# Performance work log

Measured on AMD Instinct MI355X. Metric: run time of the kernel, lower is better.

Reference implementation:

```python
import jax, jax.numpy as jnp
import numpy as np

ANNEALING_SCALE = 0.1
BS, NV, S, D, V = 2, 16, 1024, 768, 50257

def setup_inputs() -> dict:
    key = jax.random.key(0)
    k1, k2, k3, k4, k5 = jax.random.split(key, 5)
    return {
        "input_ids": jax.random.randint(k1, (BS, S), 0, V),
        "content": jax.random.normal(k2, (BS, NV, S, D), dtype=jnp.float32),
        "contextualization": jax.random.normal(k3, (BS, NV, S, S), dtype=jnp.float32) * 0.05,
        "lm_head_weight": jax.random.normal(k4, (V, D), dtype=jnp.float32) * 0.02,
        "content_weights": jax.random.uniform(k5, (V, NV), dtype=jnp.float32),
    }

def reference(input_ids, content, contextualization, lm_head_weight, content_weights):
    bs, nv, s, d = content.shape
    # --- mask_annealing ---
    # Original computes relu(content @ W.T) over full vocab then gathers at input_ids.
    # Equivalent: gather rows of W first, then contract (same math since relu is
    # elementwise and only gathered columns are summed).
    Wg = lm_head_weight[input_ids]                              # (bs, s, d)
    sims = jnp.einsum('bkid,bjd->bkij', content, Wg)            # (bs, 16, s, s)
    sims = jnp.sum(jax.nn.relu(sims), axis=3)                   # (bs, 16, s)
    scores = jax.nn.sigmoid(-ANNEALING_SCALE * sims + 6.0)
    # upweight_nearby modifier
    scores = scores * (1.0 + jnp.arange(s, dtype=content.dtype) / 100.0)[None, None, :]
    scores = jnp.transpose(scores, (0, 2, 1))                   # (bs, s, 16)
    # --- create_content_soft_mask ---
    cw = content_weights[input_ids]                             # (bs, s, 16)
    weights = cw * scores + (1.0 - scores)                      # (bs, s, 16)
    # --- weighted sense combination ---
    content_m = content * jnp.transpose(weights, (0, 2, 1))[..., None]  # (bs,16,s,d)
    hidden = jnp.einsum('bkij,bkjd->bid', contextualization, content_m) # (bs, s, d)
    logits = hidden @ lm_head_weight.T                          # (bs, s, vocab)
    return logits
```

## Files before the change

### kernel.cpp

```cpp
#include <hip/hip_runtime.h>
#include <cstdint>
#include <cstddef>

#define BSZ 2
#define NV 16
#define SEQ 1024
#define DIM 768
#define VOC 50257
#define VOCP 50304

typedef unsigned int u32;
typedef unsigned short u16;
typedef _Float16 half8 __attribute__((ext_vector_type(8)));
typedef float f32x4 __attribute__((ext_vector_type(4)));

__device__ __forceinline__ u16 f2h(float f) {
  return __builtin_bit_cast(unsigned short, (_Float16)f);
}
__device__ __forceinline__ u32 pk2h(float a, float b) {
  return (u32)f2h(a) | ((u32)f2h(b) << 16);
}

__device__ __forceinline__ void gload16(const u16* g, u16* l) {
  __builtin_amdgcn_global_load_lds(
      (const __attribute__((address_space(1))) void*)g,
      (__attribute__((address_space(3))) void*)l, 16, 0, 0);
}

__global__ void k_prep_content(const float* __restrict__ content,
                               u16* __restrict__ cbf, u16* __restrict__ cT) {
  __shared__ u16 tile[32][33];
  const int bk = blockIdx.z;
  const int d0 = blockIdx.x * 32, j0 = blockIdx.y * 32;
  const float* src = content + (size_t)bk * SEQ * DIM;
  u16* dst = cbf + (size_t)bk * SEQ * DIM;
  u16* dstT = cT + (size_t)bk * DIM * SEQ;
  const int c = threadIdx.x;
#pragma unroll
  for (int rr = 0; rr < 4; ++rr) {
    const int r = threadIdx.y * 4 + rr;
    const float v = src[(size_t)(j0 + r) * DIM + d0 + c];
    const u16 bv = f2h(v);
    dst[(size_t)(j0 + r) * DIM + d0 + c] = bv;
    tile[r][c] = bv;
  }
  __syncthreads();
#pragma unroll
  for (int rr = 0; rr < 4; ++rr) {
    const int r = threadIdx.y * 4 + rr;
    dstT[(size_t)(d0 + r) * SEQ + j0 + c] = tile[c][r];
  }
}

__global__ void k_prep_w(const float* __restrict__ W, u16* __restrict__ Wb) {
  const int v = blockIdx.x;
  const int c = threadIdx.x * 4;
  u32 lo, hi;
  if (v < VOC) {
    const float4 f = *(const float4*)(W + (size_t)v * DIM + c);
    lo = pk2h(f.x, f.y); hi = pk2h(f.z, f.w);
  } else {
    lo = 0u; hi = 0u;
  }
  *(uint2*)(Wb + (size_t)v * DIM + c) = make_uint2(lo, hi);
}

__global__ void k_gather(const int* __restrict__ ids, const u16* __restrict__ Wb,
                         u16* __restrict__ Wg) {
  const int b = blockIdx.y, j = blockIdx.x;
  const int row = ids[b * SEQ + j];
  const int c = threadIdx.x * 4;
  *(uint2*)(Wg + ((size_t)b * SEQ + j) * DIM + c) =
      *(const uint2*)(Wb + (size_t)row * DIM + c);
}

__global__ void k_zero(float* __restrict__ p, int n) {
  const int i = blockIdx.x * 256 + threadIdx.x;
  if (i < n) p[i] = 0.f;
}

template <int LDA, int LDB>
__device__ __forceinline__ void gemm_core(const u16* __restrict__ A,
                                          const u16* __restrict__ B, int ksteps,
                                          u16* As, u16* Bs, f32x4 (&acc)[4][4],
                                          int t) {
  const int lane = t & 63, w = t >> 6, wr = w >> 1, wc = w & 1;
  const int rl = lane & 15;
  const int gsw = (((lane >> 4) ^ ((rl >> 1) & 3)) * 8);
  const int srow = 16 * w + (lane >> 2);
  const int sg = (((lane & 3) ^ ((lane >> 3) & 3)) * 8);
  const size_t gaBase = (size_t)srow * LDA + sg;
  const size_t gbBase = (size_t)srow * LDB + sg;
  u16* lA = As + w * 512;
  u16* lB = Bs + w * 512;

#define STAGE_(bb, kt)                                                  \
  {                                                                     \
    const u16* ga_ = A + gaBase + (size_t)(kt) * 32;                    \
    const u16* gb_ = B + gbBase + (size_t)(kt) * 32;                    \
    gload16(ga_, lA + (bb) * 4096);                                     \
    gload16(ga_ + (size_t)64 * LDA, lA + (bb) * 4096 + 2048);           \
    gload16(gb_, lB + (bb) * 4096);                                     \
    gload16(gb_ + (size_t)64 * LDB, lB + (bb) * 4096 + 2048);           \
  }

#define FRAGS_(bb)                                                      \
  half8 af[4], bf[4];                                                   \
  _Pragma("unroll") for (int m = 0; m < 4; ++m)                         \
      af[m] = *(const half8*)(As + (bb) * 4096 +                        \
                              (wr * 64 + m * 16 + rl) * 32 + gsw);      \
  _Pragma("unroll") for (int n = 0; n < 4; ++n)                         \
      bf[n] = *(const half8*)(Bs + (bb) * 4096 +                        \
                              (wc * 64 + n * 16 + rl) * 32 + gsw);      \
  _Pragma("unroll") for (int m = 0; m < 4; ++m)                         \
      _Pragma("unroll") for (int n = 0; n < 4; ++n)                     \
          acc[m][n] = __builtin_amdgcn_mfma_f32_16x16x32_f16(           \
              af[m], bf[n], acc[m][n], 0, 0, 0);

  STAGE_(0, 0);
  __syncthreads();
  int cur = 0;
  for (int kt = 0; kt < ksteps - 1; ++kt) {
    STAGE_(cur ^ 1, kt + 1);
    { FRAGS_(cur); }
    __syncthreads();
    cur ^= 1;
  }
  { FRAGS_(cur); }
#undef STAGE_
#undef FRAGS_
}

__global__ __launch_bounds__(256) void k_sims(const u16* __restrict__ cbf,
                                              const u16* __restrict__ Wg,
                                              float* __restrict__ sims) {
  __shared__ __align__(16) u16 As[2 * 128 * 32];
  __shared__ __align__(16) u16 Bs[2 * 128 * 32];
  const int bk = blockIdx.z, b = bk >> 4;
  const int t = threadIdx.x;
  const u16* A = cbf + (size_t)bk * SEQ * DIM + (size_t)(blockIdx.y * 128) * DIM;
  const u16* B = Wg + (size_t)b * SEQ * DIM + (size_t)(blockIdx.x * 128) * DIM;
  f32x4 acc[4][4] = {};
  gemm_core<DIM, DIM>(A, B, DIM / 32, As, Bs, acc, t);
  const int lane = t & 63, w = t >> 6, wr = w >> 1;
  const int rg = lane >> 4, cl = lane & 15;
#pragma unroll
  for (int m = 0; m < 4; ++m) {
#pragma unroll
    for (int r = 0; r < 4; ++r) {
      float s = 0.f;
#pragma unroll
      for (int n = 0; n < 4; ++n) {
        const float v = acc[m][n][r];
        s += fmaxf(v, 0.f);
      }
      s += __shfl_xor(s, 1);
      s += __shfl_xor(s, 2);
      s += __shfl_xor(s, 4);
      s += __shfl_xor(s, 8);
      if (cl == 0) {
        const int i = blockIdx.y * 128 + wr * 64 + m * 16 + rg * 4 + r;
        atomicAdd(&sims[(size_t)bk * SEQ + i], s);
      }
    }
  }
}

__global__ void k_weights(const float* __restrict__ sims, const int* __restrict__ ids,
                          const float* __restrict__ cw, float* __restrict__ wtsT) {
  const int j = blockIdx.x * 256 + threadIdx.x;
  const int bk = blockIdx.y;
  const int b = bk >> 4, k = bk & 15;
  const float sm = sims[(size_t)bk * SEQ + j];
  float score = 1.f / (1.f + __expf(0.1f * sm - 6.f));
  score *= 1.f + (float)j * 0.01f;
  const int id = ids[b * SEQ + j];
  const float c = cw[(size_t)id * NV + k];
  wtsT[(size_t)bk * SEQ + j] = c * score + (1.f - score);
}

__global__ void k_ctx(const float* __restrict__ ctx, const float* __restrict__ wtsT,
                      u16* __restrict__ ctxw) {
  const size_t i = ((size_t)blockIdx.x * 256 + threadIdx.x) * 4;
  const float4 c = *(const float4*)(ctx + i);
  const size_t bk = i >> 20;
  const int j = (int)(i & (SEQ - 1));
  const float4 wv = *(const float4*)(wtsT + bk * SEQ + j);
  *(uint2*)(ctxw + i) =
      make_uint2(pk2h(c.x * wv.x, c.y * wv.y), pk2h(c.z * wv.z, c.w * wv.w));
}

__global__ __launch_bounds__(256) void k_hidden(const u16* __restrict__ ctxw,
                                                const u16* __restrict__ cT,
                                                float* __restrict__ part) {
  __shared__ __align__(16) u16 As[2 * 128 * 32];
  __shared__ __align__(16) u16 Bs[2 * 128 * 32];
  const int z = blockIdx.z;
  const int b = z >> 2, g = z & 3;
  const int i0 = blockIdx.y * 128, d0 = blockIdx.x * 128;
  const int t = threadIdx.x;
  f32x4 acc[4][4] = {};
  for (int kk = 0; kk < 4; ++kk) {
    const int sense = g * 4 + kk;
    const u16* A = ctxw + ((size_t)(b * NV + sense) * SEQ + i0) * SEQ;
    const u16* B = cT + ((size_t)(b * NV + sense) * DIM + d0) * SEQ;
    gemm_core<SEQ, SEQ>(A, B, SEQ / 32, As, Bs, acc, t);
    __syncthreads();
  }
  const int lane = t & 63, w = t >> 6, wr = w >> 1, wc = w & 1;
  const int rg = lane >> 4, cl = lane & 15;
  float* P = part + ((size_t)(g * BSZ + b) * SEQ + i0) * DIM + d0;
#pragma unroll
  for (int m = 0; m < 4; ++m)
#pragma unroll
    for (int n = 0; n < 4; ++n)
#pragma unroll
      for (int r = 0; r < 4; ++r)
        P[(size_t)(wr * 64 + m * 16 + rg * 4 + r) * DIM + wc * 64 + n * 16 + cl] =
            acc[m][n][r];
}

__global__ void k_reduce(const float* __restrict__ part, u16* __restrict__ hid) {
  const size_t i = ((size_t)blockIdx.x * 256 + threadIdx.x) * 4;
  const size_t NHID = (size_t)BSZ * SEQ * DIM;
  float4 s = {0.f, 0.f, 0.f, 0.f};
#pragma unroll
  for (int g = 0; g < 4; ++g) {
    const float4 p = *(const float4*)(part + (size_t)g * NHID + i);
    s.x += p.x; s.y += p.y; s.z += p.z; s.w += p.w;
  }
  *(uint2*)(hid + i) = make_uint2(pk2h(s.x, s.y), pk2h(s.z, s.w));
}

__global__ __launch_bounds__(256) void k_logits(const u16* __restrict__ hid,
                                                const u16* __restrict__ Wb,
                                                float* __restrict__ out) {
  __shared__ __align__(16) u16 As[2 * 128 * 32];
  __shared__ __align__(16) u16 Bs[2 * 128 * 32];
  const int nwg = 16 * 393;
  const int bid = blockIdx.x;
  const int swz = (bid & 7) * (nwg / 8) + (bid >> 3);
  const int i0 = (swz & 15) * 128, v0 = (swz >> 4) * 128;
  const int t = threadIdx.x;
  const u16* A = hid + (size_t)i0 * DIM;
  const u16* B = Wb + (size_t)v0 * DIM;
  f32x4 acc[4][4] = {};
  gemm_core<DIM, DIM>(A, B, DIM / 32, As, Bs, acc, t);
  const int lane = t & 63, w = t >> 6, wr = w >> 1, wc = w & 1;
  const int rg = lane >> 4, cl = lane & 15;
#pragma unroll
  for (int m = 0; m < 4; ++m)
#pragma unroll
    for (int n = 0; n < 4; ++n) {
      const int vv = v0 + wc * 64 + n * 16 + cl;
      if (vv < VOC) {
#pragma unroll
        for (int r = 0; r < 4; ++r) {
          const int i = i0 + wr * 64 + m * 16 + rg * 4 + r;
          out[(size_t)i * VOC + vv] = acc[m][n][r];
        }
      }
    }
}

extern "C" void kernel_launch(void* const* d_in, const int* in_sizes, int n_in,
                              void* d_out, int out_size, void* d_ws, size_t ws_size,
                              hipStream_t stream) {
  const int* ids = (const int*)d_in[0];
  const float* content = (const float*)d_in[1];
  const float* ctx = (const float*)d_in[2];
  const float* W = (const float*)d_in[3];
  const float* cw = (const float*)d_in[4];
  float* out = (float*)d_out;
  char* ws = (char*)d_ws;

  u16* cbf  = (u16*)(ws);
  u16* cT   = (u16*)(ws + 50331648);
  u16* Wb   = (u16*)(ws + 100663296);
  u16* Wg   = (u16*)(ws + 177930240);
  u16* ctxw = (u16*)(ws + 181075968);
  float* sims = (float*)(ws + 248184832);
  float* wtsT = (float*)(ws + 248315904);
  float* part = (float*)cbf;
  u16* hid = Wg;

  k_prep_content<<<dim3(DIM / 32, SEQ / 32, BSZ * NV), dim3(32, 8), 0, stream>>>(
      content, cbf, cT);
  k_prep_w<<<VOCP, 192, 0, stream>>>(W, Wb);
  k_gather<<<dim3(SEQ, BSZ), 192, 0, stream>>>(ids, Wb, Wg);
  k_zero<<<128, 256, 0, stream>>>(sims, BSZ * NV * SEQ);
  k_sims<<<dim3(8, 8, BSZ * NV), 256, 0, stream>>>(cbf, Wg, sims);
  k_weights<<<dim3(4, BSZ * NV), 256, 0, stream>>>(sims, ids, cw, wtsT);
  k_ctx<<<32768, 256, 0, stream>>>(ctx, wtsT, ctxw);
  k_hidden<<<dim3(6, 8, 8), 256, 0, stream>>>(ctxw, cT, part);
  k_reduce<<<1536, 256, 0, stream>>>(part, hid);
  k_logits<<<16 * 393, 256, 0, stream>>>(hid, Wb, out);
}
```

Baseline: 634.5 us.

## Rewrite logits GEMM with 256x256 tiles, 4-stage LDS pipeline, 512 threads

The logits GEMM moves from 128x128 tiles on 256 threads to 256x256 tiles on 512 threads. It adds a 4-buffer LDS ring fed by direct global-to-LDS loads with explicit vmcnt waits, XOR-swizzled LDS addressing, s_setprio around the MFMA bursts, and nontemporal output stores. The last vocab tile overlaps the previous one to avoid going out of bounds. The aim is more data reuse per tile, better overlap of loads with MFMA, and less cache pollution from the large fp32 output, at the cost of 128 KB of LDS and only one workgroup per CU.

```diff
diff --git a/kernel.cpp b/kernel.cpp
--- a/kernel.cpp
+++ b/kernel.cpp
@@ -232,33 +232,96 @@
   *(uint2*)(hid + i) = make_uint2(pk2h(s.x, s.y), pk2h(s.z, s.w));
 }
 
-__global__ __launch_bounds__(256) void k_logits(const u16* __restrict__ hid,
+__global__ __launch_bounds__(512) void k_logits(const u16* __restrict__ hid,
                                                 const u16* __restrict__ Wb,
                                                 float* __restrict__ out) {
-  __shared__ __align__(16) u16 As[2 * 128 * 32];
-  __shared__ __align__(16) u16 Bs[2 * 128 * 32];
-  const int nwg = 16 * 393;
+  __shared__ __align__(16) u16 lds[65536];
   const int bid = blockIdx.x;
-  const int swz = (bid & 7) * (nwg / 8) + (bid >> 3);
-  const int i0 = (swz & 15) * 128, v0 = (swz >> 4) * 128;
+  const int swz = (bid & 7) * 197 + (bid >> 3);
+  const int vt = swz >> 3, it = swz & 7;
+  const int i0 = it * 256;
+  const int v0 = (vt == 196) ? (VOCP - 256) : vt * 256;
   const int t = threadIdx.x;
-  const u16* A = hid + (size_t)i0 * DIM;
-  const u16* B = Wb + (size_t)v0 * DIM;
-  f32x4 acc[4][4] = {};
-  gemm_core<DIM, DIM>(A, B, DIM / 32, As, Bs, acc, t);
-  const int lane = t & 63, w = t >> 6, wr = w >> 1, wc = w & 1;
-  const int rg = lane >> 4, cl = lane & 15;
-#pragma unroll
-  for (int m = 0; m < 4; ++m)
+  const int lane = t & 63, w = t >> 6;
+  const int wm = w >> 2, wn = w & 3;
+  const int rl = lane & 15, kg = lane >> 4;
+  const int gsw = ((kg ^ ((rl >> 1) & 3))) * 8;
+  const int aoff = (wm * 128 + rl) * 32 + gsw;
+  const int boff = 8192 + (wn * 64 + rl) * 32 + gsw;
+  const int srow = t >> 2;
+  const int sgg = ((t & 3) ^ ((t >> 3) & 3)) * 8;
+  const u16* gA0 = hid + (size_t)(i0 + srow) * DIM + sgg;
+  const u16* gA1 = hid + (size_t)(i0 + 128 + srow) * DIM + sgg;
+  const u16* gB0 = Wb + (size_t)(v0 + srow) * DIM + sgg;
+  const u16* gB1 = Wb + (size_t)(v0 + 128 + srow) * DIM + sgg;
+  const int wb = w * 512;
+
+#define STG_A(tt)                                              \
+  {                                                            \
+    u16* d_ = lds + ((tt) & 3) * 16384 + wb;                   \
+    gload16(gA0 + (size_t)(tt) * 32, d_);                      \
+    gload16(gA1 + (size_t)(tt) * 32, d_ + 4096);               \
+  }
+#define STG_B(tt)                                              \
+  {                                                            \
+    u16* d_ = lds + ((tt) & 3) * 16384 + 8192 + wb;            \
+    gload16(gB0 + (size_t)(tt) * 32, d_);                      \
+    gload16(gB1 + (size_t)(tt) * 32, d_ + 4096);               \
+  }
+
+  f32x4 acc[8][4] = {};
+  STG_A(0); STG_B(0); STG_A(1); STG_B(1); STG_A(2); STG_B(2);
+  for (int tt = 0; tt < 24; ++tt) {
+    if (tt < 22)
+      asm volatile("s_waitcnt vmcnt(8)" ::: "memory");
+    else if (tt == 22)
+      asm volatile("s_waitcnt vmcnt(4)" ::: "memory");
+    else
+      asm volatile("s_waitcnt vmcnt(0)" ::: "memory");
+    __builtin_amdgcn_s_barrier();
+    __builtin_amdgcn_sched_barrier(0);
+    const u16* bp = lds + (tt & 3) * 16384;
+    half8 af[4], bf[4];
+#pragma unroll
+    for (int n = 0; n < 4; ++n) bf[n] = *(const half8*)(bp + boff + n * 512);
+#pragma unroll
+    for (int m = 0; m < 4; ++m) af[m] = *(const half8*)(bp + aoff + m * 512);
+    if (tt + 3 < 24) STG_A(tt + 3);
+    __builtin_amdgcn_s_setprio(1);
+#pragma unroll
+    for (int m = 0; m < 4; ++m)
+#pragma unroll
+      for (int n = 0; n < 4; ++n)
+        acc[m][n] =
+            __builtin_amdgcn_mfma_f32_16x16x32_f16(af[m], bf[n], acc[m][n], 0, 0, 0);
+    __builtin_amdgcn_s_setprio(0);
+    __builtin_amdgcn_s_barrier();
+#pragma unroll
+    for (int m = 0; m < 4; ++m)
+      af[m] = *(const half8*)(bp + aoff + 2048 + m * 512);
+    if (tt + 3 < 24) STG_B(tt + 3);
+    __builtin_amdgcn_s_setprio(1);
+#pragma unroll
+    for (int m = 0; m < 4; ++m)
+#pragma unroll
+      for (int n = 0; n < 4; ++n)
+        acc[4 + m][n] =
+            __builtin_amdgcn_mfma_f32_16x16x32_f16(af[m], bf[n], acc[4 + m][n], 0, 0, 0);
+    __builtin_amdgcn_s_setprio(0);
+  }
+#undef STG_A
+#undef STG_B
+#pragma unroll
+  for (int m = 0; m < 8; ++m)
 #pragma unroll
     for (int n = 0; n < 4; ++n) {
-      const int vv = v0 + wc * 64 + n * 16 + cl;
-      if (vv < VOC) {
-#pragma unroll
-        for (int r = 0; r < 4; ++r) {
-          const int i = i0 + wr * 64 + m * 16 + rg * 4 + r;
-          out[(size_t)i * VOC + vv] = acc[m][n][r];
-        }
+      const int v = v0 + wn * 64 + n * 16 + rl;
+      if (v < VOC) {
+        const int ib = i0 + wm * 128 + m * 16 + kg * 4;
+#pragma unroll
+        for (int r = 0; r < 4; ++r)
+          __builtin_nontemporal_store(acc[m][n][r],
+                                      &out[(size_t)(ib + r) * VOC + v]);
       }
     }
 }
@@ -294,5 +357,5 @@
   k_ctx<<<32768, 256, 0, stream>>>(ctx, wtsT, ctxw);
   k_hidden<<<dim3(6, 8, 8), 256, 0, stream>>>(ctxw, cT, part);
   k_reduce<<<1536, 256, 0, stream>>>(part, hid);
-  k_logits<<<16 * 393, 256, 0, stream>>>(hid, Wb, out);
-}
+  k_logits<<<8 * 197, 512, 0, stream>>>(hid, Wb, out);
+}
```

Measured after the change: 795.3 us. +25.4%, slower.

## Enlarge GEMM tiles to 256x128 in sims and logits kernels

Applied to the files above, without the earlier changes.

Adds a gemm_core2 variant in which each workgroup computes two 128-row A tiles against one shared B tile, doubling each wave's accumulators. k_sims and k_logits switch to it, which halves their grid sizes and the number of times B tiles are loaded from global memory and LDS, giving more MFMA work per B load. The cost is higher register pressure (two 4x4 f32x4 accumulator sets) and more LDS per block, which may limit occupancy despite launch_bounds(256,2), and fewer blocks for the sims grid.

```diff
diff --git a/kernel.cpp b/kernel.cpp
--- a/kernel.cpp
+++ b/kernel.cpp
@@ -131,36 +131,105 @@
 #undef FRAGS_
 }
 
-__global__ __launch_bounds__(256) void k_sims(const u16* __restrict__ cbf,
-                                              const u16* __restrict__ Wg,
-                                              float* __restrict__ sims) {
-  __shared__ __align__(16) u16 As[2 * 128 * 32];
+template <int LDA, int LDB>
+__device__ __forceinline__ void gemm_core2(const u16* __restrict__ A0,
+                                           const u16* __restrict__ A1,
+                                           const u16* __restrict__ B, int ksteps,
+                                           u16* As0, u16* As1, u16* Bs,
+                                           f32x4 (&acc0)[4][4],
+                                           f32x4 (&acc1)[4][4], int t) {
+  const int lane = t & 63, w = t >> 6, wr = w >> 1, wc = w & 1;
+  const int rl = lane & 15;
+  const int gsw = (((lane >> 4) ^ ((rl >> 1) & 3)) * 8);
+  const int srow = 16 * w + (lane >> 2);
+  const int sg = (((lane & 3) ^ ((lane >> 3) & 3)) * 8);
+  const size_t gaBase = (size_t)srow * LDA + sg;
+  const size_t gbBase = (size_t)srow * LDB + sg;
+  u16* lA0 = As0 + w * 512;
+  u16* lA1 = As1 + w * 512;
+  u16* lB = Bs + w * 512;
+
+#define STAGE2_(bb, kt)                                                 \
+  {                                                                     \
+    const u16* ga0_ = A0 + gaBase + (size_t)(kt) * 32;                  \
+    const u16* ga1_ = A1 + gaBase + (size_t)(kt) * 32;                  \
+    const u16* gb_ = B + gbBase + (size_t)(kt) * 32;                    \
+    gload16(ga0_, lA0 + (bb) * 4096);                                   \
+    gload16(ga0_ + (size_t)64 * LDA, lA0 + (bb) * 4096 + 2048);         \
+    gload16(ga1_, lA1 + (bb) * 4096);                                   \
+    gload16(ga1_ + (size_t)64 * LDA, lA1 + (bb) * 4096 + 2048);         \
+    gload16(gb_, lB + (bb) * 4096);                                     \
+    gload16(gb_ + (size_t)64 * LDB, lB + (bb) * 4096 + 2048);           \
+  }
+
+#define FRAGS2_(bb)                                                     \
+  half8 af0[4], af1[4], bf[4];                                          \
+  _Pragma("unroll") for (int n = 0; n < 4; ++n)                         \
+      bf[n] = *(const half8*)(Bs + (bb) * 4096 +                        \
+                              (wc * 64 + n * 16 + rl) * 32 + gsw);      \
+  _Pragma("unroll") for (int m = 0; m < 4; ++m)                         \
+      af0[m] = *(const half8*)(As0 + (bb) * 4096 +                      \
+                               (wr * 64 + m * 16 + rl) * 32 + gsw);     \
+  _Pragma("unroll") for (int m = 0; m < 4; ++m)                         \
+      af1[m] = *(const half8*)(As1 + (bb) * 4096 +                      \
+                               (wr * 64 + m * 16 + rl) * 32 + gsw);     \
+  _Pragma("unroll") for (int m = 0; m < 4; ++m)                         \
+      _Pragma("unroll") for (int n = 0; n < 4; ++n)                     \
+          acc0[m][n] = __builtin_amdgcn_mfma_f32_16x16x32_f16(          \
+              af0[m], bf[n], acc0[m][n], 0, 0, 0);                      \
+  _Pragma("unroll") for (int m = 0; m < 4; ++m)                         \
+      _Pragma("unroll") for (int n = 0; n < 4; ++n)                     \
+          acc1[m][n] = __builtin_amdgcn_mfma_f32_16x16x32_f16(          \
+              af1[m], bf[n], acc1[m][n], 0, 0, 0);
+
+  STAGE2_(0, 0);
+  __syncthreads();
+  int cur = 0;
+  for (int kt = 0; kt < ksteps - 1; ++kt) {
+    STAGE2_(cur ^ 1, kt + 1);
+    { FRAGS2_(cur); }
+    __syncthreads();
+    cur ^= 1;
+  }
+  { FRAGS2_(cur); }
+#undef STAGE2_
+#undef FRAGS2_
+}
+
+__global__ __launch_bounds__(256, 2) void k_sims(const u16* __restrict__ cbf,
+                                                 const u16* __restrict__ Wg,
+                                                 float* __restrict__ sims) {
+  __shared__ __align__(16) u16 As0[2 * 128 * 32];
+  __shared__ __align__(16) u16 As1[2 * 128 * 32];
   __shared__ __align__(16) u16 Bs[2 * 128 * 32];
   const int bk = blockIdx.z, b = bk >> 4;
   const int t = threadIdx.x;
-  const u16* A = cbf + (size_t)bk * SEQ * DIM + (size_t)(blockIdx.y * 128) * DIM;
+  const int i0 = blockIdx.y * 256;
+  const u16* A0 = cbf + (size_t)bk * SEQ * DIM + (size_t)i0 * DIM;
+  const u16* A1 = A0 + (size_t)128 * DIM;
   const u16* B = Wg + (size_t)b * SEQ * DIM + (size_t)(blockIdx.x * 128) * DIM;
-  f32x4 acc[4][4] = {};
-  gemm_core<DIM, DIM>(A, B, DIM / 32, As, Bs, acc, t);
+  f32x4 acc0[4][4] = {}, acc1[4][4] = {};
+  gemm_core2<DIM, DIM>(A0, A1, B, DIM / 32, As0, As1, Bs, acc0, acc1, t);
   const int lane = t & 63, w = t >> 6, wr = w >> 1;
   const int rg = lane >> 4, cl = lane & 15;
 #pragma unroll
   for (int m = 0; m < 4; ++m) {
 #pragma unroll
     for (int r = 0; r < 4; ++r) {
-      float s = 0.f;
+      float s0 = 0.f, s1 = 0.f;
 #pragma unroll
       for (int n = 0; n < 4; ++n) {
-        const float v = acc[m][n][r];
-        s += fmaxf(v, 0.f);
+        s0 += fmaxf(acc0[m][n][r], 0.f);
+        s1 += fmaxf(acc1[m][n][r], 0.f);
       }
-      s += __shfl_xor(s, 1);
-      s += __shfl_xor(s, 2);
-      s += __shfl_xor(s, 4);
-      s += __shfl_xor(s, 8);
+      s0 += __shfl_xor(s0, 1); s1 += __shfl_xor(s1, 1);
+      s0 += __shfl_xor(s0, 2); s1 += __shfl_xor(s1, 2);
+      s0 += __shfl_xor(s0, 4); s1 += __shfl_xor(s1, 4);
+      s0 += __shfl_xor(s0, 8); s1 += __shfl_xor(s1, 8);
       if (cl == 0) {
-        const int i = blockIdx.y * 128 + wr * 64 + m * 16 + rg * 4 + r;
-        atomicAdd(&sims[(size_t)bk * SEQ + i], s);
+        const int i = i0 + wr * 64 + m * 16 + rg * 4 + r;
+        atomicAdd(&sims[(size_t)bk * SEQ + i], s0);
+        atomicAdd(&sims[(size_t)bk * SEQ + i + 128], s1);
       }
     }
   }
@@ -232,20 +301,22 @@
   *(uint2*)(hid + i) = make_uint2(pk2h(s.x, s.y), pk2h(s.z, s.w));
 }
 
-__global__ __launch_bounds__(256) void k_logits(const u16* __restrict__ hid,
-                                                const u16* __restrict__ Wb,
-                                                float* __restrict__ out) {
-  __shared__ __align__(16) u16 As[2 * 128 * 32];
+__global__ __launch_bounds__(256, 2) void k_logits(const u16* __restrict__ hid,
+                                                   const u16* __restrict__ Wb,
+                                                   float* __restrict__ out) {
+  __shared__ __align__(16) u16 As0[2 * 128 * 32];
+  __shared__ __align__(16) u16 As1[2 * 128 * 32];
   __shared__ __align__(16) u16 Bs[2 * 128 * 32];
-  const int nwg = 16 * 393;
   const int bid = blockIdx.x;
-  const int swz = (bid & 7) * (nwg / 8) + (bid >> 3);
-  const int i0 = (swz & 15) * 128, v0 = (swz >> 4) * 128;
+  const int swz = (bid & 7) * 393 + (bid >> 3);
+  const int it = swz & 7, vt = swz >> 3;
+  const int i0 = it * 256, v0 = vt * 128;
   const int t = threadIdx.x;
-  const u16* A = hid + (size_t)i0 * DIM;
+  const u16* A0 = hid + (size_t)i0 * DIM;
+  const u16* A1 = A0 + (size_t)128 * DIM;
   const u16* B = Wb + (size_t)v0 * DIM;
-  f32x4 acc[4][4] = {};
-  gemm_core<DIM, DIM>(A, B, DIM / 32, As, Bs, acc, t);
+  f32x4 acc0[4][4] = {}, acc1[4][4] = {};
+  gemm_core2<DIM, DIM>(A0, A1, B, DIM / 32, As0, As1, Bs, acc0, acc1, t);
   const int lane = t & 63, w = t >> 6, wr = w >> 1, wc = w & 1;
   const int rg = lane >> 4, cl = lane & 15;
 #pragma unroll
@@ -254,11 +325,13 @@
     for (int n = 0; n < 4; ++n) {
       const int vv = v0 + wc * 64 + n * 16 + cl;
       if (vv < VOC) {
-#pragma unroll
-        for (int r = 0; r < 4; ++r) {
-          const int i = i0 + wr * 64 + m * 16 + rg * 4 + r;
-          out[(size_t)i * VOC + vv] = acc[m][n][r];
-        }
+        const int i = i0 + wr * 64 + m * 16 + rg * 4;
+#pragma unroll
+        for (int r = 0; r < 4; ++r)
+          out[(size_t)(i + r) * VOC + vv] = acc0[m][n][r];
+#pragma unroll
+        for (int r = 0; r < 4; ++r)
+          out[(size_t)(i + 128 + r) * VOC + vv] = acc1[m][n][r];
       }
     }
 }
@@ -289,10 +362,10 @@
   k_prep_w<<<VOCP, 192, 0, stream>>>(W, Wb);
   k_gather<<<dim3(SEQ, BSZ), 192, 0, stream>>>(ids, Wb, Wg);
   k_zero<<<128, 256, 0, stream>>>(sims, BSZ * NV * SEQ);
-  k_sims<<<dim3(8, 8, BSZ * NV), 256, 0, stream>>>(cbf, Wg, sims);
+  k_sims<<<dim3(8, 4, BSZ * NV), 256, 0, stream>>>(cbf, Wg, sims);
   k_weights<<<dim3(4, BSZ * NV), 256, 0, stream>>>(sims, ids, cw, wtsT);
   k_ctx<<<32768, 256, 0, stream>>>(ctx, wtsT, ctxw);
   k_hidden<<<dim3(6, 8, 8), 256, 0, stream>>>(ctxw, cT, part);
   k_reduce<<<1536, 256, 0, stream>>>(part, hid);
-  k_logits<<<16 * 393, 256, 0, stream>>>(hid, Wb, out);
-}
+  k_logits<<<8 * 393, 256, 0, stream>>>(hid, Wb, out);
+}
```

Result: no change. 639.2 us (+0.8%).
